# Optimization experiments

Hardware: AMD Instinct MI355X
Metric: run time of the kernel (lower is better)

## Reference

```python
import jax, jax.numpy as jnp
import numpy as np


def setup_inputs() -> dict:
    key = jax.random.key(0)
    ks = jax.random.split(key, 32)
    def rn(i, shape, s=0.02):
        return jax.random.normal(ks[i], shape, dtype=jnp.float32) * s
    z = lambda n: jnp.zeros((n,), dtype=jnp.float32)
    return {
        'c2': rn(0, (8, 256, 112, 112), 1.0),
        'c3': rn(1, (8, 512, 56, 56), 1.0),
        'c4': rn(2, (8, 1024, 28, 28), 1.0),
        'c5': rn(3, (8, 2048, 14, 14), 1.0),
        'lat_w0': rn(4, (256, 256)),  'lat_b0': z(256),
        'lat_w1': rn(5, (512, 256)),  'lat_b1': z(256),
        'lat_w2': rn(6, (1024, 256)), 'lat_b2': z(256),
        'lat_w3': rn(7, (2048, 256)), 'lat_b3': z(256),
        'sp_w1': rn(8, (2048, 512)), 'sp_b1': z(512),
        'sp_w2': rn(9, (512, 4)),    'sp_b2': z(4),
        'qkv_w': rn(10, (256, 768)), 'qkv_b': z(768),
        'proj_w': rn(11, (256, 256)), 'proj_b': z(256),
        'gat_W': rn(12, (4, 256, 256)),
        'gat_a': rn(13, (4, 512)),
        'out_w': rn(14, (1024, 256)), 'out_b': z(256),
        'label_emb': rn(15, (80, 256), 1.0),
        'spec_w1': rn(16, (256, 128)), 'spec_b1': z(128),
        'spec_w2': rn(17, (128, 80)),  'spec_b2': z(80),
        'spat_w1': rn(18, (256, 128)), 'spat_b1': z(128),
        'spat_w2': rn(19, (128, 80)),  'spat_b2': z(80),
        'gate_w': rn(20, (256, 80)), 'gate_b': z(80),
        'unc_w': rn(21, (256, 80)),  'unc_b': z(80),
    }


def _forward(c2, c3, c4, c5,
             lat_w0, lat_b0, lat_w1, lat_b1, lat_w2, lat_b2, lat_w3, lat_b3,
             sp_w1, sp_b1, sp_w2, sp_b2,
             qkv_w, qkv_b, proj_w, proj_b,
             gat_W, gat_a, out_w, out_b, label_emb,
             spec_w1, spec_b1, spec_w2, spec_b2,
             spat_w1, spat_b1, spat_w2, spat_b2,
             gate_w, gate_b, unc_w, unc_b):
    B = c2.shape[0]
    L = label_emb.shape[0]
    C = 256
    # --- DynamicScaleAwareFPN ---
    pooled = c5.mean(axis=(2, 3))                                   # [B,2048]
    sw = jax.nn.softmax(jax.nn.relu(pooled @ sp_w1 + sp_b1) @ sp_w2 + sp_b2, axis=1)  # [B,4]
    H, W = c2.shape[2], c2.shape[3]
    feats = (c2, c3, c4, c5)
    lws = (lat_w0, lat_w1, lat_w2, lat_w3)
    lbs = (lat_b0, lat_b1, lat_b2, lat_b3)
    fused = jnp.zeros((B, C, H, W), dtype=c2.dtype)
    for i in range(4):  # fixed 4 scales
        l = jnp.einsum('bchw,cd->bdhw', feats[i], lws[i]) + lbs[i][None, :, None, None]
        if l.shape[2] != H or l.shape[3] != W:
            l = jax.image.resize(l, (B, C, H, W), method='bilinear')  # align_corners=False
        fused = fused + l * sw[:, i, None, None, None]
    # --- DeformableAttention (N=H*W > max_tokens=196 -> adaptive pool to 14x14) ---
    th = 14
    x = fused.reshape(B, C, th, H // th, th, W // th).mean(axis=(3, 5))  # exact adaptive avg pool
    x = x.reshape(B, C, th * th).transpose(0, 2, 1)                      # [B,196,C]
    N, nh, hd = th * th, 8, C // 8
    qkv = (x @ qkv_w + qkv_b).reshape(B, N, 3, nh, hd).transpose(2, 0, 3, 1, 4)
    q, k, v = qkv[0], qkv[1], qkv[2]                                     # [B,nh,N,hd]
    attn = jax.nn.softmax(jnp.einsum('bhnd,bhmd->bhnm', q, k) * (hd ** -0.5), axis=-1)
    xo = jnp.einsum('bhnm,bhmd->bhnd', attn, v).transpose(0, 2, 1, 3).reshape(B, N, C)
    xo = xo @ proj_w + proj_b
    gctx = xo.mean(axis=1)                                               # [B,C]
    # --- CrossLabelSemanticGraph (4 GAT heads) ---
    lf = label_emb[None] + gctx[:, None, :]                              # [B,L,C]
    def gat(Wm, avec):
        Wx = lf @ Wm                                                     # [B,L,C]
        # a([Wx_i ; Wx_j]) = Wx_i @ a1 + Wx_j @ a2  (avoids O(L^2*2C) tensor)
        s1 = Wx @ avec[:C]                                               # [B,L]
        s2 = Wx @ avec[C:]                                               # [B,L]
        e = jax.nn.leaky_relu(s1[:, :, None] + s2[:, None, :], 0.2)      # [B,L,L]
        att = jax.nn.softmax(e, axis=2)
        return att @ Wx, att
    heads, atts = jax.vmap(gat)(gat_W, gat_a)                            # [4,B,L,C],[4,B,L,L]
    concat = jnp.moveaxis(heads, 0, 2).reshape(B, L, 4 * C)              # head-order concat
    graph = concat @ out_w + out_b                                       # [B,L,C]
    agg = graph.mean(axis=1)                                             # [B,C]
    # --- SpectralSpatialFusion (dropout inactive at eval) ---
    spec = jax.nn.relu(agg @ spec_w1 + spec_b1) @ spec_w2 + spec_b2
    spat = jax.nn.relu(agg @ spat_w1 + spat_b1) @ spat_w2 + spat_b2
    gate = jax.nn.sigmoid(agg @ gate_w + gate_b)
    logits = gate * spec + (1.0 - gate) * spat
    # --- UncertaintyHead ---
    alpha = jax.nn.softplus(agg @ unc_w + unc_b) + 1.0
    unc = L / jnp.sum(alpha, axis=1, keepdims=True)
    return (logits, spec, spat, gate, unc, sw, atts)


def reference(c2, c3, c4, c5,
              lat_w0, lat_b0, lat_w1, lat_b1, lat_w2, lat_b2, lat_w3, lat_b3,
              sp_w1, sp_b1, sp_w2, sp_b2,
              qkv_w, qkv_b, proj_w, proj_b,
              gat_W, gat_a, out_w, out_b, label_emb,
              spec_w1, spec_b1, spec_w2, spec_b2,
              spat_w1, spat_b1, spat_w2, spat_b2,
              gate_w, gate_b, unc_w, unc_b):
    return _forward(c2, c3, c4, c5,
                    lat_w0, lat_b0, lat_w1, lat_b1, lat_w2, lat_b2, lat_w3, lat_b3,
                    sp_w1, sp_b1, sp_w2, sp_b2,
                    qkv_w, qkv_b, proj_w, proj_b,
                    gat_W, gat_a, out_w, out_b, label_emb,
                    spec_w1, spec_b1, spec_w2, spec_b2,
                    spat_w1, spat_b1, spat_w2, spat_b2,
                    gate_w, gate_b, unc_w, unc_b)
```

## Files before the change

kernel.cpp:

```cpp
#include <hip/hip_runtime.h>
#include <math.h>

typedef __attribute__((ext_vector_type(8))) short bshort8;
typedef __attribute__((ext_vector_type(4))) float f32x4;

#define DI __device__ __forceinline__

DI unsigned short f2bf(float x) {
    unsigned int u = __builtin_bit_cast(unsigned int, x);
    u += 0x7fffu + ((u >> 16) & 1u);
    return (unsigned short)(u >> 16);
}

DI bshort8 pack8(const float* v) {
    bshort8 r;
    #pragma unroll
    for (int j = 0; j < 8; j++) r[j] = (short)f2bf(v[j]);
    return r;
}

DI f32x4 mfma16(bshort8 a, bshort8 b, f32x4 c) {
    return __builtin_amdgcn_mfma_f32_16x16x32_bf16(a, b, c, 0, 0, 0);
}

__device__ const float W14[14][3] = {
    {0.875f, 0.125f, 0.f},
    {0.125f, 0.75f, 0.125f}, {0.125f, 0.75f, 0.125f}, {0.125f, 0.75f, 0.125f},
    {0.125f, 0.75f, 0.125f}, {0.125f, 0.75f, 0.125f}, {0.125f, 0.75f, 0.125f},
    {0.125f, 0.75f, 0.125f}, {0.125f, 0.75f, 0.125f}, {0.125f, 0.75f, 0.125f},
    {0.125f, 0.75f, 0.125f}, {0.125f, 0.75f, 0.125f}, {0.125f, 0.75f, 0.125f},
    {0.125f, 0.875f, 0.f}};
__device__ const float W28[14][4] = {
    {0.5f, 0.4375f, 0.0625f, 0.f},
    {0.0625f, 0.4375f, 0.4375f, 0.0625f}, {0.0625f, 0.4375f, 0.4375f, 0.0625f},
    {0.0625f, 0.4375f, 0.4375f, 0.0625f}, {0.0625f, 0.4375f, 0.4375f, 0.0625f},
    {0.0625f, 0.4375f, 0.4375f, 0.0625f}, {0.0625f, 0.4375f, 0.4375f, 0.0625f},
    {0.0625f, 0.4375f, 0.4375f, 0.0625f}, {0.0625f, 0.4375f, 0.4375f, 0.0625f},
    {0.0625f, 0.4375f, 0.4375f, 0.0625f}, {0.0625f, 0.4375f, 0.4375f, 0.0625f},
    {0.0625f, 0.4375f, 0.4375f, 0.0625f}, {0.0625f, 0.4375f, 0.4375f, 0.0625f},
    {0.0625f, 0.4375f, 0.5f, 0.f}};
__device__ const float W56[14][6] = {
    {0.25f, 0.25f, 0.25f, 0.21875f, 0.03125f, 0.f},
    {0.03125f, 0.21875f, 0.25f, 0.25f, 0.21875f, 0.03125f},
    {0.03125f, 0.21875f, 0.25f, 0.25f, 0.21875f, 0.03125f},
    {0.03125f, 0.21875f, 0.25f, 0.25f, 0.21875f, 0.03125f},
    {0.03125f, 0.21875f, 0.25f, 0.25f, 0.21875f, 0.03125f},
    {0.03125f, 0.21875f, 0.25f, 0.25f, 0.21875f, 0.03125f},
    {0.03125f, 0.21875f, 0.25f, 0.25f, 0.21875f, 0.03125f},
    {0.03125f, 0.21875f, 0.25f, 0.25f, 0.21875f, 0.03125f},
    {0.03125f, 0.21875f, 0.25f, 0.25f, 0.21875f, 0.03125f},
    {0.03125f, 0.21875f, 0.25f, 0.25f, 0.21875f, 0.03125f},
    {0.03125f, 0.21875f, 0.25f, 0.25f, 0.21875f, 0.03125f},
    {0.03125f, 0.21875f, 0.25f, 0.25f, 0.21875f, 0.03125f},
    {0.03125f, 0.21875f, 0.25f, 0.25f, 0.21875f, 0.03125f},
    {0.03125f, 0.21875f, 0.25f, 0.25f, 0.25f, 0.f}};

template <int N, int C, int TAPS>
DI void pool_body(const float* __restrict__ src, float* __restrict__ dst,
                  unsigned blk, unsigned t)
{
    unsigned id = blk * 256u + t;
    unsigned p = id / 196u;
    unsigned r = id - p * 196u;
    unsigned ti = r / 14u, tj = r - ti * 14u;
    unsigned b = p / C, cin = p - b * C;
    const float* plane = src + (size_t)p * (N * N);
    float acc = 0.f;
    if constexpr (N == 112) {
        const float4* p4 = (const float4*)(plane + (size_t)(ti * 8) * 112 + tj * 8);
        #pragma unroll
        for (int i = 0; i < 8; i++) {
            float4 u = p4[i * 28];
            float4 v = p4[i * 28 + 1];
            acc += (u.x + u.y) + (u.z + u.w) + (v.x + v.y) + (v.z + v.w);
        }
        acc *= (1.f / 64.f);
    } else {
        constexpr int STRIDE = N / 14;
        const float (*WT)[TAPS] = (N == 14) ? (const float (*)[TAPS])W14
                                : (N == 28) ? (const float (*)[TAPS])W28
                                            : (const float (*)[TAPS])W56;
        int hs = (int)(STRIDE * ti) - 1; if (hs < 0) hs = 0;
        int ws = (int)(STRIDE * tj) - 1; if (ws < 0) ws = 0;
        float wh[TAPS], ww[TAPS];
        #pragma unroll
        for (int i = 0; i < TAPS; i++) { wh[i] = WT[ti][i]; ww[i] = WT[tj][i]; }
        #pragma unroll
        for (int i = 0; i < TAPS; i++) {
            int hi = hs + i; if (hi > N - 1) hi = N - 1;
            const float* row = plane + (size_t)hi * N;
            float rs = 0.f;
            #pragma unroll
            for (int j = 0; j < TAPS; j++) {
                int wj = ws + j; if (wj > N - 1) wj = N - 1;
                rs += ww[j] * row[wj];
            }
            acc += wh[i] * rs;
        }
    }
    dst[(size_t)cin * 1568 + b * 196 + r] = acc;
}

DI void c5_mean_body(const float* __restrict__ c5, float* __restrict__ pooled,
                     unsigned blk, unsigned t)
{
    int wid = t >> 6, lane = t & 63;
    int p = blk * 4 + wid;
    const float* plane = c5 + (size_t)p * 196;
    float v = plane[lane] + plane[64 + lane] + plane[128 + lane];
    if (lane < 4) v += plane[192 + lane];
    #pragma unroll
    for (int off = 32; off > 0; off >>= 1) v += __shfl_xor(v, off, 64);
    if (lane == 0) pooled[p] = v * (1.f / 196.f);
}

__global__ __launch_bounds__(256) void pool_all(
    const float* __restrict__ c2, const float* __restrict__ c3,
    const float* __restrict__ c4, const float* __restrict__ c5,
    float* __restrict__ pf0, float* __restrict__ pf1,
    float* __restrict__ pf2, float* __restrict__ pf3,
    float* __restrict__ pooled)
{
    unsigned bx = blockIdx.x, t = threadIdx.x;
    if (bx < 1568u)       pool_body<112, 256, 8>(c2, pf0, bx, t);
    else if (bx < 4704u)  pool_body<56, 512, 6>(c3, pf1, bx - 1568u, t);
    else if (bx < 10976u) pool_body<28, 1024, 4>(c4, pf2, bx - 4704u, t);
    else if (bx < 23520u) pool_body<14, 2048, 3>(c5, pf3, bx - 10976u, t);
    else                  c5_mean_body(c5, pooled, bx - 23520u, t);
}

__global__ __launch_bounds__(512) void sw_part(
    const float* __restrict__ pooled, const float* __restrict__ sp_w1,
    float* __restrict__ partial,
    const float* __restrict__ gat_W, const float* __restrict__ gat_a,
    float* __restrict__ Wa)
{
    int t = threadIdx.x;
    if (blockIdx.y >= 8) {
        int e = (blockIdx.y - 8) * 8 + blockIdx.x;
        int h = e >> 2, q = e & 3;
        __shared__ float a1[256], a2[256];
        if (t < 256) { a1[t] = gat_a[h * 512 + t]; a2[t] = gat_a[h * 512 + 256 + t]; }
        __syncthreads();
        int w = t >> 6, lane = t & 63;
        #pragma unroll
        for (int ci = 0; ci < 8; ci++) {
            int c = q * 64 + w * 8 + ci;
            const float* row = gat_W + (size_t)h * 65536 + (size_t)c * 256;
            float p1 = 0.f, p2 = 0.f;
            #pragma unroll
            for (int jj = 0; jj < 4; jj++) {
                float v = row[lane + 64 * jj];
                p1 += v * a1[lane + 64 * jj];
                p2 += v * a2[lane + 64 * jj];
            }
            #pragma unroll
            for (int off = 32; off > 0; off >>= 1) {
                p1 += __shfl_xor(p1, off, 64);
                p2 += __shfl_xor(p2, off, 64);
            }
            if (lane == 0) { Wa[h * 512 + c] = p1; Wa[h * 512 + 256 + c] = p2; }
        }
        return;
    }
    int b = blockIdx.x, kc = blockIdx.y;
    __shared__ float ps[256];
    if (t < 256) ps[t] = pooled[b * 2048 + kc * 256 + t];
    __syncthreads();
    float acc = 0.f;
    const float* w = sp_w1 + (size_t)(kc * 256) * 512 + t;
    #pragma unroll 8
    for (int c = 0; c < 256; c++) acc += ps[c] * w[(size_t)c * 512];
    partial[((size_t)b * 8 + kc) * 512 + t] = acc;
}

__global__ __launch_bounds__(512) void sw_fin(
    const float* __restrict__ partial, const float* __restrict__ sp_b1,
    const float* __restrict__ sp_w2, const float* __restrict__ sp_b2,
    const float* __restrict__ lb0, const float* __restrict__ lb1,
    const float* __restrict__ lb2, const float* __restrict__ lb3,
    const float* __restrict__ lemb, const float* __restrict__ Wa,
    float* __restrict__ sw_out, float* __restrict__ xtok,
    float* __restrict__ ldot)
{
    int b = blockIdx.x, t = threadIdx.x;
    __shared__ float h[512];
    __shared__ float s4s[4];
    __shared__ float swl[4];
    __shared__ float bf_s[256];
    float a = sp_b1[t];
    #pragma unroll
    for (int kc = 0; kc < 8; kc++) a += partial[((size_t)b * 8 + kc) * 512 + t];
    h[t] = fmaxf(a, 0.f);
    __syncthreads();
    int wv = t >> 6, lane = t & 63;
    if (wv < 4) {
        float acc = 0.f;
        #pragma unroll
        for (int i = 0; i < 8; i++) {
            int idx = lane + 64 * i;
            acc += h[idx] * sp_w2[idx * 4 + wv];
        }
        #pragma unroll
        for (int off = 32; off > 0; off >>= 1) acc += __shfl_xor(acc, off, 64);
        if (lane == 0) s4s[wv] = acc + sp_b2[wv];
    }
    __syncthreads();
    if (t == 0) {
        float mx = fmaxf(fmaxf(s4s[0], s4s[1]), fmaxf(s4s[2], s4s[3]));
        float e0 = expf(s4s[0] - mx), e1 = expf(s4s[1] - mx);
        float e2 = expf(s4s[2] - mx), e3 = expf(s4s[3] - mx);
        float inv = 1.f / (e0 + e1 + e2 + e3);
        swl[0] = e0 * inv; swl[1] = e1 * inv; swl[2] = e2 * inv; swl[3] = e3 * inv;
        for (int o = 0; o < 4; o++) sw_out[b * 4 + o] = swl[o];
    }
    __syncthreads();
    if (t < 256)
        bf_s[t] = swl[0] * lb0[t] + swl[1] * lb1[t] + swl[2] * lb2[t] + swl[3] * lb3[t];
    {
        int pair = t >> 6;
        #pragma unroll
        for (int r = 0; r < 10; r++) {
            int l = b * 10 + r;
            const float* le = lemb + l * 256 + lane * 4;
            const float* wa = Wa + pair * 256 + lane * 4;
            float p = le[0] * wa[0] + le[1] * wa[1] + le[2] * wa[2] + le[3] * wa[3];
            #pragma unroll
            for (int off = 32; off > 0; off >>= 1) p += __shfl_xor(p, off, 64);
            if (lane == 0) ldot[l * 8 + pair] = p;
        }
    }
    __syncthreads();
    int c = t & 255, half = t >> 8;
    float bv = bf_s[c];
    float* xb = xtok + (size_t)b * 196 * 256 + c;
    for (int r = half; r < 196; r += 2) xb[(size_t)r * 256] = bv;
}

__global__ __launch_bounds__(256) void lateral_slice(
    const float* __restrict__ pf0, const float* __restrict__ pf1,
    const float* __restrict__ pf2, const float* __restrict__ pf3,
    const float* __restrict__ w0, const float* __restrict__ w1,
    const float* __restrict__ w2, const float* __restrict__ w3,
    const float* __restrict__ sw, float* __restrict__ xtok)
{
    const int sArr[8]    = {0, 1, 2, 2, 3, 3, 3, 3};
    const int koffArr[8] = {0, 0, 0, 512, 0, 512, 1024, 1536};
    const int klenArr[8] = {256, 512, 512, 512, 512, 512, 512, 512};
    int sl = blockIdx.y;
    int s = sArr[sl], koff = koffArr[sl], klen = klenArr[sl];
    const float* pf = (s == 0) ? pf0 : (s == 1) ? pf1 : (s == 2) ? pf2 : pf3;
    const float* W  = (s == 0) ? w0  : (s == 1) ? w1  : (s == 2) ? w2  : w3;

    int mt = blockIdx.x % 49, nt = blockIdx.x / 49;
    int m0 = mt * 32, n0 = nt * 64;
    __shared__ alignas(16) unsigned short As[1024];
    __shared__ alignas(16) unsigned short Bs[2048];
    int t = threadIdx.x, lane = t & 63, wid = t >> 6;
    int wm = wid >> 1, wn = wid & 1;
    f32x4 acc0 = {0, 0, 0, 0}, acc1 = {0, 0, 0, 0};

    int f = t & 63;
    int mA = m0 + ((t >> 6) & 1) * 16 + (f & 15);
    int kbA = (f >> 4) * 8;
    int nB = n0 + (t >> 6) * 16 + (f & 15);
    int kbB = (f >> 4) * 8;
    float swv = sw[(mA / 196) * 4 + s];

    float ar[8], br[8];
    auto loadA = [&](int k0) {
        if (t < 128) {
            const float* base = pf + (size_t)(koff + k0 + kbA) * 1568 + mA;
            #pragma unroll
            for (int j = 0; j < 8; j++) ar[j] = base[(size_t)j * 1568] * swv;
        }
    };
    auto loadB = [&](int k0) {
        const float* base = W + (size_t)(koff + k0 + kbB) * 256 + nB;
        #pragma unroll
        for (int j = 0; j < 8; j++) br[j] = base[(size_t)j * 256];
    };

    loadA(0); loadB(0);
    for (int k0 = 0; k0 < klen; k0 += 32) {
        if (t < 128) *(bshort8*)&As[(((t >> 6) & 1) * 512 + f * 8)] = pack8(ar);
        *(bshort8*)&Bs[((t >> 6) * 512 + f * 8)] = pack8(br);
        __syncthreads();
        if (k0 + 32 < klen) { loadA(k0 + 32); loadB(k0 + 32); }
        bshort8 av = *(const bshort8*)&As[wm * 512 + lane * 8];
        bshort8 bv0 = *(const bshort8*)&Bs[(wn * 2 + 0) * 512 + lane * 8];
        bshort8 bv1 = *(const bshort8*)&Bs[(wn * 2 + 1) * 512 + lane * 8];
        acc0 = mfma16(av, bv0, acc0);
        acc1 = mfma16(av, bv1, acc1);
        __syncthreads();
    }
    int col0 = n0 + wn * 32 + (lane & 15);
    int rbase = m0 + wm * 16 + ((lane >> 4) << 2);
    #pragma unroll
    for (int r = 0; r < 4; r++) {
        int m = rbase + r;
        atomicAdd(&xtok[(size_t)m * 256 + col0], acc0[r]);
        atomicAdd(&xtok[(size_t)m * 256 + col0 + 16], acc1[r]);
    }
}

template <bool B_IS_KXN>
__global__ __launch_bounds__(256) void gemm_kernel(
    const float* __restrict__ Ab, int lda, long long sAy, long long sAz,
    const float* __restrict__ Bb, int ldb, long long sBy, long long sBz,
    float* __restrict__ Cb, int ldc, long long sCy, long long sCz,
    const float* __restrict__ bias, int M, int N, int K,
    float alpha, int mtiles)
{
    const float* A = Ab + blockIdx.y * sAy + blockIdx.z * sAz;
    const float* B = Bb + blockIdx.y * sBy + blockIdx.z * sBz;
    float* C = Cb + blockIdx.y * sCy + blockIdx.z * sCz;
    int mt = blockIdx.x % mtiles, nt = blockIdx.x / mtiles;
    int m0 = mt * 32, n0 = nt * 64;
    __shared__ alignas(16) unsigned short As[1024];
    __shared__ alignas(16) unsigned short Bs[2048];
    int t = threadIdx.x, lane = t & 63, wid = t >> 6;
    int wm = wid >> 1, wn = wid & 1;
    f32x4 acc0 = {0, 0, 0, 0}, acc1 = {0, 0, 0, 0};

    int f = t & 63;
    int mA = m0 + ((t >> 6) & 1) * 16 + (f & 15);
    int kbA = (f >> 4) * 8;
    int nB = n0 + (t >> 6) * 16 + (f & 15);
    int kbB = (f >> 4) * 8;

    float ar[8], br[8];
    auto loadA = [&](int k0) {
        if (t < 128) {
            int kb = k0 + kbA;
            if (mA < M && kb + 8 <= K) {
                const float4* p = (const float4*)(A + (size_t)mA * lda + kb);
                float4 u = p[0], v = p[1];
                ar[0] = u.x; ar[1] = u.y; ar[2] = u.z; ar[3] = u.w;
                ar[4] = v.x; ar[5] = v.y; ar[6] = v.z; ar[7] = v.w;
            } else {
                #pragma unroll
                for (int j = 0; j < 8; j++) {
                    int k = kb + j;
                    ar[j] = (mA < M && k < K) ? A[(size_t)mA * lda + k] : 0.f;
                }
            }
        }
    };
    auto loadB = [&](int k0) {
        int kb = k0 + kbB;
        if constexpr (B_IS_KXN) {
            #pragma unroll
            for (int j = 0; j < 8; j++) {
                int k = kb + j;
                br[j] = (k < K && nB < N) ? B[(size_t)k * ldb + nB] : 0.f;
            }
        } else {
            if (nB < N && kb + 8 <= K) {
                const float4* p = (const float4*)(B + (size_t)nB * ldb + kb);
                float4 u = p[0], v = p[1];
                br[0] = u.x; br[1] = u.y; br[2] = u.z; br[3] = u.w;
                br[4] = v.x; br[5] = v.y; br[6] = v.z; br[7] = v.w;
            } else {
                #pragma unroll
                for (int j = 0; j < 8; j++) {
                    int k = kb + j;
                    br[j] = (nB < N && k < K) ? B[(size_t)nB * ldb + k] : 0.f;
                }
            }
        }
    };

    loadA(0); loadB(0);
    for (int k0 = 0; k0 < K; k0 += 32) {
        if (t < 128) *(bshort8*)&As[(((t >> 6) & 1) * 512 + f * 8)] = pack8(ar);
        *(bshort8*)&Bs[((t >> 6) * 512 + f * 8)] = pack8(br);
        __syncthreads();
        if (k0 + 32 < K) { loadA(k0 + 32); loadB(k0 + 32); }
        bshort8 av = *(const bshort8*)&As[wm * 512 + lane * 8];
        bshort8 bv0 = *(const bshort8*)&Bs[(wn * 2 + 0) * 512 + lane * 8];
        bshort8 bv1 = *(const bshort8*)&Bs[(wn * 2 + 1) * 512 + lane * 8];
        acc0 = mfma16(av, bv0, acc0);
        acc1 = mfma16(av, bv1, acc1);
        __syncthreads();
    }
    int col0 = n0 + wn * 32 + (lane & 15);
    int rbase = m0 + wm * 16 + ((lane >> 4) << 2);
    #pragma unroll
    for (int r = 0; r < 4; r++) {
        int m = rbase + r;
        if (m < M) {
            if (col0 < N) {
                float v = acc0[r] * alpha;
                if (bias) v += bias[col0];
                C[(size_t)m * ldc + col0] = v;
            }
            int c1 = col0 + 16;
            if (c1 < N) {
                float v = acc1[r] * alpha;
                if (bias) v += bias[c1];
                C[(size_t)m * ldc + c1] = v;
            }
        }
    }
}

__global__ __launch_bounds__(256) void attn_softmax(float* __restrict__ S)
{
    int wid = threadIdx.x >> 6, lane = threadIdx.x & 63;
    size_t row = (size_t)blockIdx.x * 4 + wid;
    float* p = S + row * 196;
    float v0 = p[lane];
    float v1 = p[64 + lane];
    float v2 = p[128 + lane];
    float v3 = (lane < 4) ? p[192 + lane] : -1e30f;
    float mx = fmaxf(fmaxf(v0, v1), fmaxf(v2, v3));
    #pragma unroll
    for (int off = 32; off > 0; off >>= 1) mx = fmaxf(mx, __shfl_xor(mx, off, 64));
    float e0 = expf(v0 - mx), e1 = expf(v1 - mx), e2 = expf(v2 - mx);
    float e3 = (lane < 4) ? expf(v3 - mx) : 0.f;
    float sum = e0 + e1 + e2 + e3;
    #pragma unroll
    for (int off = 32; off > 0; off >>= 1) sum += __shfl_xor(sum, off, 64);
    float inv = 1.f / sum;
    p[lane] = e0 * inv;
    p[64 + lane] = e1 * inv;
    p[128 + lane] = e2 * inv;
    if (lane < 4) p[192 + lane] = e3 * inv;
}

__global__ __launch_bounds__(1024) void tail1(
    const float* __restrict__ xo, const float* __restrict__ proj_w,
    const float* __restrict__ proj_b,
    const float* __restrict__ gat_W, const float* __restrict__ lemb,
    const float* __restrict__ Wa, const float* __restrict__ ldot,
    float* __restrict__ atts, float* __restrict__ hm_g)
{
    int b = blockIdx.x >> 2, h = blockIdx.x & 3;
    int t = threadIdx.x, lane = t & 63, wv = t >> 6;
    __shared__ float red[1024];
    __shared__ float xm[256];
    __shared__ float gctx_s[256];
    __shared__ float gdot_s[2];
    __shared__ float s12h[160];
    __shared__ float am_s[80];
    __shared__ float av_s[256];

    {
        int c = t & 255, sl = t >> 8;
        const float* base = xo + ((size_t)b * 196 + sl * 49) * 256 + c;
        float s = 0.f;
        #pragma unroll 7
        for (int i = 0; i < 49; i++) s += base[(size_t)i * 256];
        red[t] = s;
    }
    if (t < 80) am_s[t] = 0.f;
    __syncthreads();
    if (t < 256) xm[t] = (red[t] + red[256 + t] + red[512 + t] + red[768 + t]) * (1.f / 196.f);
    __syncthreads();

    {
        int n = t & 255, ks = t >> 8;
        float acc = 0.f;
        const float* w = proj_w + (size_t)(ks * 64) * 256 + n;
        #pragma unroll 8
        for (int i = 0; i < 64; i++) acc += xm[ks * 64 + i] * w[(size_t)i * 256];
        red[t] = acc;
    }
    __syncthreads();
    if (t < 256) gctx_s[t] = proj_b[t] + red[t] + red[256 + t] + red[512 + t] + red[768 + t];
    __syncthreads();

    if (wv < 2) {
        int pair = h * 2 + wv;
        const float* wa = Wa + pair * 256 + lane * 4;
        float p = gctx_s[lane * 4] * wa[0] + gctx_s[lane * 4 + 1] * wa[1]
                + gctx_s[lane * 4 + 2] * wa[2] + gctx_s[lane * 4 + 3] * wa[3];
        #pragma unroll
        for (int off = 32; off > 0; off >>= 1) p += __shfl_xor(p, off, 64);
        if (lane == 0) gdot_s[wv] = p;
    }
    __syncthreads();
    if (t < 160) {
        int q = t / 80, l = t - q * 80;
        s12h[t] = ldot[l * 8 + h * 2 + q] + gdot_s[q];
    }
    __syncthreads();

    {
        #pragma unroll
        for (int rr = 0; rr < 5; rr++) {
            int i = rr * 16 + wv;
            float s1i = s12h[i];
            const float* s2 = s12h + 80;
            float v0 = s1i + s2[lane]; v0 = v0 > 0.f ? v0 : 0.2f * v0;
            float v1 = -1e30f;
            if (lane < 16) { v1 = s1i + s2[64 + lane]; v1 = v1 > 0.f ? v1 : 0.2f * v1; }
            float mx = fmaxf(v0, v1);
            #pragma unroll
            for (int off = 32; off > 0; off >>= 1) mx = fmaxf(mx, __shfl_xor(mx, off, 64));
            float e0 = expf(v0 - mx), e1 = (lane < 16) ? expf(v1 - mx) : 0.f;
            float sum = e0 + e1;
            #pragma unroll
            for (int off = 32; off > 0; off >>= 1) sum += __shfl_xor(sum, off, 64);
            float inv = 1.f / sum;
            float* orow = atts + (size_t)h * 51200 + b * 6400 + i * 80;
            float p0 = e0 * inv;
            orow[lane] = p0;
            atomicAdd(&am_s[lane], p0);
            if (lane < 16) {
                float p1 = e1 * inv;
                orow[64 + lane] = p1;
                atomicAdd(&am_s[64 + lane], p1);
            }
        }
    }
    __syncthreads();

    {
        int n = t & 255, ks = t >> 8;
        float acc = 0.f;
        const float* le = lemb + n;
        #pragma unroll 5
        for (int l = ks * 20; l < ks * 20 + 20; l++) acc += am_s[l] * le[(size_t)l * 256];
        red[t] = acc;
    }
    __syncthreads();
    if (t < 256)
        av_s[t] = (red[t] + red[256 + t] + red[512 + t] + red[768 + t]) * (1.f / 80.f)
                + gctx_s[t];
    __syncthreads();
    {
        int n = t & 255, ks = t >> 8;
        float acc = 0.f;
        const float* w = gat_W + (size_t)h * 65536 + (size_t)(ks * 64) * 256 + n;
        #pragma unroll 8
        for (int i = 0; i < 64; i++) acc += av_s[ks * 64 + i] * w[(size_t)i * 256];
        red[t] = acc;
    }
    __syncthreads();
    if (t < 256)
        hm_g[(b * 4 + h) * 256 + t] = red[t] + red[256 + t] + red[512 + t] + red[768 + t];
}

__global__ __launch_bounds__(1024) void tail2(
    const float* __restrict__ hm_g,
    const float* __restrict__ out_w, const float* __restrict__ out_b,
    const float* __restrict__ spec_w1, const float* __restrict__ spec_b1,
    const float* __restrict__ spec_w2, const float* __restrict__ spec_b2,
    const float* __restrict__ spat_w1, const float* __restrict__ spat_b1,
    const float* __restrict__ spat_w2, const float* __restrict__ spat_b2,
    const float* __restrict__ gate_w, const float* __restrict__ gate_b,
    const float* __restrict__ unc_w, const float* __restrict__ unc_b,
    float* __restrict__ out)
{
    int b = blockIdx.x, t = threadIdx.x;
    __shared__ float red[1024];
    __shared__ float as_s[256];
    __shared__ float hb_s[256];
    __shared__ float fv_s[320];

    {
        int n = t & 255, ks = t >> 8;
        float acc = 0.f;
        const float* hv = hm_g + b * 1024 + ks * 256;
        const float* w = out_w + (size_t)(ks * 256) * 256 + n;
        #pragma unroll 8
        for (int k = 0; k < 256; k++) acc += hv[k] * w[(size_t)k * 256];
        red[t] = acc;
    }
    __syncthreads();
    if (t < 256) as_s[t] = out_b[t] + red[t] + red[256 + t] + red[512 + t] + red[768 + t];
    __syncthreads();

    {
        int u = t & 255, ks = t >> 8;
        int which = u >> 7, oo = u & 127;
        const float* w1 = which ? spat_w1 : spec_w1;
        float acc = 0.f;
        #pragma unroll 8
        for (int i = 0; i < 64; i++) {
            int k = ks * 64 + i;
            acc += as_s[k] * w1[(size_t)k * 128 + oo];
        }
        red[t] = acc;
    }
    __syncthreads();
    if (t < 256) {
        int which = t >> 7, oo = t & 127;
        const float* b1 = which ? spat_b1 : spec_b1;
        hb_s[t] = fmaxf(red[t] + red[256 + t] + red[512 + t] + red[768 + t] + b1[oo], 0.f);
    }
    __syncthreads();

    if (t < 960) {
        int sub = t / 320, u = t - sub * 320;
        int head = u / 80, o = u - head * 80;
        const float* wp; const float* src; int K;
        if (head == 0)      { wp = spec_w2; src = hb_s;       K = 128; }
        else if (head == 1) { wp = spat_w2; src = hb_s + 128; K = 128; }
        else if (head == 2) { wp = gate_w;  src = as_s;       K = 256; }
        else                { wp = unc_w;   src = as_s;       K = 256; }
        int k0 = (K * sub) / 3, k1 = (K * (sub + 1)) / 3;
        float acc = 0.f;
        for (int k = k0; k < k1; k++) acc += src[k] * wp[(size_t)k * 80 + o];
        red[sub * 320 + u] = acc;
    }
    __syncthreads();
    if (t < 320) {
        int head = t / 80, o = t - head * 80;
        const float* bp = head == 0 ? spec_b2 : head == 1 ? spat_b2 : head == 2 ? gate_b : unc_b;
        fv_s[t] = red[t] + red[320 + t] + red[640 + t] + bp[o];
    }
    __syncthreads();

    if (t < 80) {
        float sp = fv_s[t], st2 = fv_s[80 + t], gz = fv_s[160 + t], uz = fv_s[240 + t];
        float g = 1.f / (1.f + expf(-gz));
        out[b * 80 + t] = g * sp + (1.f - g) * st2;
        out[640 + b * 80 + t] = sp;
        out[1280 + b * 80 + t] = st2;
        out[1920 + b * 80 + t] = g;
        red[t] = log1pf(expf(uz)) + 1.f;
    }
    __syncthreads();
    if (t == 0) {
        float s = 0.f;
        for (int l = 0; l < 80; l++) s += red[l];
        out[2560 + b] = 80.f / s;
    }
}

extern "C" void kernel_launch(void* const* d_in, const int* in_sizes, int n_in,
                              void* d_out, int out_size, void* d_ws, size_t ws_size,
                              hipStream_t stream)
{
    (void)in_sizes; (void)n_in; (void)out_size; (void)ws_size;
    const float* c2 = (const float*)d_in[0];
    const float* c3 = (const float*)d_in[1];
    const float* c4 = (const float*)d_in[2];
    const float* c5 = (const float*)d_in[3];
    const float* lat_w0 = (const float*)d_in[4];
    const float* lat_b0 = (const float*)d_in[5];
    const float* lat_w1 = (const float*)d_in[6];
    const float* lat_b1 = (const float*)d_in[7];
    const float* lat_w2 = (const float*)d_in[8];
    const float* lat_b2 = (const float*)d_in[9];
    const float* lat_w3 = (const float*)d_in[10];
    const float* lat_b3 = (const float*)d_in[11];
    const float* sp_w1 = (const float*)d_in[12];
    const float* sp_b1 = (const float*)d_in[13];
    const float* sp_w2 = (const float*)d_in[14];
    const float* sp_b2 = (const float*)d_in[15];
    const float* qkv_w = (const float*)d_in[16];
    const float* qkv_b = (const float*)d_in[17];
    const float* proj_w = (const float*)d_in[18];
    const float* proj_b = (const float*)d_in[19];
    const float* gat_W = (const float*)d_in[20];
    const float* gat_a = (const float*)d_in[21];
    const float* out_w = (const float*)d_in[22];
    const float* out_b = (const float*)d_in[23];
    const float* label_emb = (const float*)d_in[24];
    const float* spec_w1 = (const float*)d_in[25];
    const float* spec_b1 = (const float*)d_in[26];
    const float* spec_w2 = (const float*)d_in[27];
    const float* spec_b2 = (const float*)d_in[28];
    const float* spat_w1 = (const float*)d_in[29];
    const float* spat_b1 = (const float*)d_in[30];
    const float* spat_w2 = (const float*)d_in[31];
    const float* spat_b2 = (const float*)d_in[32];
    const float* gate_w = (const float*)d_in[33];
    const float* gate_b = (const float*)d_in[34];
    const float* unc_w = (const float*)d_in[35];
    const float* unc_b = (const float*)d_in[36];

    float* out = (float*)d_out;
    float* ws = (float*)d_ws;

    float* pf0    = ws + 0;
    float* pf1    = ws + 401408;
    float* pf2    = ws + 1204224;
    float* pf3    = ws + 2809856;
    float* pooled = ws + 6021120;
    float* swpart = ws + 6039552;
    float* Wa     = ws + 6072320;
    float* ldot   = ws + 6074368;
    float* qkv    = ws + 0;
    float* S      = ws + 1204224;
    float* xo     = ws + 3662848;
    float* hm_g   = ws + 4253696;
    float* xtok   = ws + 6106112;

    float* swp  = out + 2568;
    float* atts = out + 2600;

    pool_all<<<27616, 256, 0, stream>>>(c2, c3, c4, c5, pf0, pf1, pf2, pf3, pooled);
    sw_part<<<dim3(8, 10), 512, 0, stream>>>(pooled, sp_w1, swpart, gat_W, gat_a, Wa);
    sw_fin<<<8, 512, 0, stream>>>(swpart, sp_b1, sp_w2, sp_b2,
                                  lat_b0, lat_b1, lat_b2, lat_b3,
                                  label_emb, Wa, swp, xtok, ldot);
    lateral_slice<<<dim3(196, 8), 256, 0, stream>>>(pf0, pf1, pf2, pf3,
                                                    lat_w0, lat_w1, lat_w2, lat_w3,
                                                    swp, xtok);
    gemm_kernel<true><<<dim3(49 * 12, 1, 1), 256, 0, stream>>>(
        xtok, 256, 0, 0, qkv_w, 768, 0, 0, qkv, 768, 0, 0,
        qkv_b, 1568, 768, 256, 1.f, 49);
    gemm_kernel<false><<<dim3(7 * 4, 8, 8), 256, 0, stream>>>(
        qkv, 768, 150528, 32, qkv + 256, 768, 150528, 32,
        S, 196, 307328, 38416, nullptr, 196, 196, 32, 0.17677669529663687f, 7);
    attn_softmax<<<3136, 256, 0, stream>>>(S);
    gemm_kernel<true><<<dim3(7, 8, 8), 256, 0, stream>>>(
        S, 196, 307328, 38416, qkv + 512, 768, 150528, 32,
        xo, 256, 50176, 32, nullptr, 196, 32, 196, 1.f, 7);
    tail1<<<32, 1024, 0, stream>>>(xo, proj_w, proj_b, gat_W, label_emb,
                                   Wa, ldot, atts, hm_g);
    tail2<<<8, 1024, 0, stream>>>(hm_g, out_w, out_b,
                                  spec_w1, spec_b1, spec_w2, spec_b2,
                                  spat_w1, spat_b1, spat_w2, spat_b2,
                                  gate_w, gate_b, unc_w, unc_b, out);
}
```

Before: 507.2 us.

## Fuse attention into one kernel and store pooled features as bf16

Measured after the change: 494.1 us. 2.6% less time.

```diff
diff --git a/kernel.cpp b/kernel.cpp
--- a/kernel.cpp
+++ b/kernel.cpp
@@ -56,7 +56,7 @@
     {0.03125f, 0.21875f, 0.25f, 0.25f, 0.25f, 0.f}};
 
 template <int N, int C, int TAPS>
-DI void pool_body(const float* __restrict__ src, float* __restrict__ dst,
+DI void pool_body(const float* __restrict__ src, unsigned short* __restrict__ dst,
                   unsigned blk, unsigned t)
 {
     unsigned id = blk * 256u + t;
@@ -68,12 +68,11 @@
     float acc = 0.f;
     if constexpr (N == 112) {
         const float4* p4 = (const float4*)(plane + (size_t)(ti * 8) * 112 + tj * 8);
-        #pragma unroll
-        for (int i = 0; i < 8; i++) {
-            float4 u = p4[i * 28];
-            float4 v = p4[i * 28 + 1];
-            acc += (u.x + u.y) + (u.z + u.w) + (v.x + v.y) + (v.z + v.w);
-        }
+        float4 rv[16];
+        #pragma unroll
+        for (int i = 0; i < 8; i++) { rv[2 * i] = p4[i * 28]; rv[2 * i + 1] = p4[i * 28 + 1]; }
+        #pragma unroll
+        for (int i = 0; i < 16; i++) acc += (rv[i].x + rv[i].y) + (rv[i].z + rv[i].w);
         acc *= (1.f / 64.f);
     } else {
         constexpr int STRIDE = N / 14;
@@ -85,20 +84,26 @@
         float wh[TAPS], ww[TAPS];
         #pragma unroll
         for (int i = 0; i < TAPS; i++) { wh[i] = WT[ti][i]; ww[i] = WT[tj][i]; }
+        float rv[TAPS][TAPS];
         #pragma unroll
         for (int i = 0; i < TAPS; i++) {
             int hi = hs + i; if (hi > N - 1) hi = N - 1;
             const float* row = plane + (size_t)hi * N;
-            float rs = 0.f;
             #pragma unroll
             for (int j = 0; j < TAPS; j++) {
                 int wj = ws + j; if (wj > N - 1) wj = N - 1;
-                rs += ww[j] * row[wj];
-            }
+                rv[i][j] = row[wj];
+            }
+        }
+        #pragma unroll
+        for (int i = 0; i < TAPS; i++) {
+            float rs = 0.f;
+            #pragma unroll
+            for (int j = 0; j < TAPS; j++) rs += ww[j] * rv[i][j];
             acc += wh[i] * rs;
         }
     }
-    dst[(size_t)cin * 1568 + b * 196 + r] = acc;
+    dst[(size_t)cin * 1568 + b * 196 + r] = f2bf(acc);
 }
 
 DI void c5_mean_body(const float* __restrict__ c5, float* __restrict__ pooled,
@@ -117,8 +122,8 @@
 __global__ __launch_bounds__(256) void pool_all(
     const float* __restrict__ c2, const float* __restrict__ c3,
     const float* __restrict__ c4, const float* __restrict__ c5,
-    float* __restrict__ pf0, float* __restrict__ pf1,
-    float* __restrict__ pf2, float* __restrict__ pf3,
+    unsigned short* __restrict__ pf0, unsigned short* __restrict__ pf1,
+    unsigned short* __restrict__ pf2, unsigned short* __restrict__ pf3,
     float* __restrict__ pooled)
 {
     unsigned bx = blockIdx.x, t = threadIdx.x;
@@ -238,8 +243,8 @@
 }
 
 __global__ __launch_bounds__(256) void lateral_slice(
-    const float* __restrict__ pf0, const float* __restrict__ pf1,
-    const float* __restrict__ pf2, const float* __restrict__ pf3,
+    const unsigned short* __restrict__ pf0, const unsigned short* __restrict__ pf1,
+    const unsigned short* __restrict__ pf2, const unsigned short* __restrict__ pf3,
     const float* __restrict__ w0, const float* __restrict__ w1,
     const float* __restrict__ w2, const float* __restrict__ w3,
     const float* __restrict__ sw, float* __restrict__ xtok)
@@ -249,7 +254,7 @@
     const int klenArr[8] = {256, 512, 512, 512, 512, 512, 512, 512};
     int sl = blockIdx.y;
     int s = sArr[sl], koff = koffArr[sl], klen = klenArr[sl];
-    const float* pf = (s == 0) ? pf0 : (s == 1) ? pf1 : (s == 2) ? pf2 : pf3;
+    const unsigned short* pf = (s == 0) ? pf0 : (s == 1) ? pf1 : (s == 2) ? pf2 : pf3;
     const float* W  = (s == 0) ? w0  : (s == 1) ? w1  : (s == 2) ? w2  : w3;
 
     int mt = blockIdx.x % 49, nt = blockIdx.x / 49;
@@ -265,14 +270,14 @@
     int kbA = (f >> 4) * 8;
     int nB = n0 + (t >> 6) * 16 + (f & 15);
     int kbB = (f >> 4) * 8;
-    float swv = sw[(mA / 196) * 4 + s];
-
-    float ar[8], br[8];
+
+    unsigned short ark[8];
+    float br[8];
     auto loadA = [&](int k0) {
         if (t < 128) {
-            const float* base = pf + (size_t)(koff + k0 + kbA) * 1568 + mA;
-            #pragma unroll
-            for (int j = 0; j < 8; j++) ar[j] = base[(size_t)j * 1568] * swv;
+            const unsigned short* base = pf + (size_t)(koff + k0 + kbA) * 1568 + mA;
+            #pragma unroll
+            for (int j = 0; j < 8; j++) ark[j] = base[(size_t)j * 1568];
         }
     };
     auto loadB = [&](int k0) {
@@ -283,7 +288,12 @@
 
     loadA(0); loadB(0);
     for (int k0 = 0; k0 < klen; k0 += 32) {
-        if (t < 128) *(bshort8*)&As[(((t >> 6) & 1) * 512 + f * 8)] = pack8(ar);
+        if (t < 128) {
+            bshort8 v8;
+            #pragma unroll
+            for (int j = 0; j < 8; j++) v8[j] = (short)ark[j];
+            *(bshort8*)&As[(((t >> 6) & 1) * 512 + f * 8)] = v8;
+        }
         *(bshort8*)&Bs[((t >> 6) * 512 + f * 8)] = pack8(br);
         __syncthreads();
         if (k0 + 32 < klen) { loadA(k0 + 32); loadB(k0 + 32); }
@@ -299,8 +309,9 @@
     #pragma unroll
     for (int r = 0; r < 4; r++) {
         int m = rbase + r;
-        atomicAdd(&xtok[(size_t)m * 256 + col0], acc0[r]);
-        atomicAdd(&xtok[(size_t)m * 256 + col0 + 16], acc1[r]);
+        float swv = sw[(m / 196) * 4 + s];
+        atomicAdd(&xtok[(size_t)m * 256 + col0], acc0[r] * swv);
+        atomicAdd(&xtok[(size_t)m * 256 + col0 + 16], acc1[r] * swv);
     }
 }
 
@@ -405,28 +416,148 @@
     }
 }
 
-__global__ __launch_bounds__(256) void attn_softmax(float* __restrict__ S)
-{
-    int wid = threadIdx.x >> 6, lane = threadIdx.x & 63;
-    size_t row = (size_t)blockIdx.x * 4 + wid;
-    float* p = S + row * 196;
-    float v0 = p[lane];
-    float v1 = p[64 + lane];
-    float v2 = p[128 + lane];
-    float v3 = (lane < 4) ? p[192 + lane] : -1e30f;
-    float mx = fmaxf(fmaxf(v0, v1), fmaxf(v2, v3));
-    #pragma unroll
-    for (int off = 32; off > 0; off >>= 1) mx = fmaxf(mx, __shfl_xor(mx, off, 64));
-    float e0 = expf(v0 - mx), e1 = expf(v1 - mx), e2 = expf(v2 - mx);
-    float e3 = (lane < 4) ? expf(v3 - mx) : 0.f;
-    float sum = e0 + e1 + e2 + e3;
-    #pragma unroll
-    for (int off = 32; off > 0; off >>= 1) sum += __shfl_xor(sum, off, 64);
-    float inv = 1.f / sum;
-    p[lane] = e0 * inv;
-    p[64 + lane] = e1 * inv;
-    p[128 + lane] = e2 * inv;
-    if (lane < 4) p[192 + lane] = e3 * inv;
+__global__ __launch_bounds__(256) void fused_attn(
+    const float* __restrict__ qkv, float* __restrict__ xo)
+{
+    int mt = blockIdx.x, h = blockIdx.y, b = blockIdx.z;
+    const float* Qb = qkv + (size_t)b * 150528 + h * 32;
+    const float* Kb = Qb + 256;
+    const float* Vb = Qb + 512;
+
+    __shared__ alignas(16) unsigned short As[1024];
+    __shared__ alignas(16) unsigned short Bs[2048];
+    __shared__ float Ss[32 * 256];
+
+    int t = threadIdx.x, lane = t & 63, wid = t >> 6;
+    int wm = wid >> 1, wn = wid & 1;
+    int f = t & 63;
+    int m0 = mt * 32;
+
+    if (t < 128) {
+        float ar[8];
+        int mA = m0 + ((t >> 6) & 1) * 16 + (f & 15);
+        int kb = (f >> 4) * 8;
+        if (mA < 196) {
+            const float4* p = (const float4*)(Qb + (size_t)mA * 768 + kb);
+            float4 u = p[0], v = p[1];
+            ar[0] = u.x; ar[1] = u.y; ar[2] = u.z; ar[3] = u.w;
+            ar[4] = v.x; ar[5] = v.y; ar[6] = v.z; ar[7] = v.w;
+        } else {
+            #pragma unroll
+            for (int j = 0; j < 8; j++) ar[j] = 0.f;
+        }
+        *(bshort8*)&As[(((t >> 6) & 1) * 512 + f * 8)] = pack8(ar);
+    }
+
+    {
+        int nBl = (t >> 6) * 16 + (f & 15);
+        int kbB = (f >> 4) * 8;
+        float br[8];
+        auto loadB = [&](int g) {
+            int key = g * 64 + nBl;
+            if (key < 196) {
+                const float4* p = (const float4*)(Kb + (size_t)key * 768 + kbB);
+                float4 u = p[0], v = p[1];
+                br[0] = u.x; br[1] = u.y; br[2] = u.z; br[3] = u.w;
+                br[4] = v.x; br[5] = v.y; br[6] = v.z; br[7] = v.w;
+            } else {
+                #pragma unroll
+                for (int j = 0; j < 8; j++) br[j] = 0.f;
+            }
+        };
+        loadB(0);
+        for (int g = 0; g < 4; g++) {
+            __syncthreads();
+            *(bshort8*)&Bs[((t >> 6) * 512 + f * 8)] = pack8(br);
+            __syncthreads();
+            if (g < 3) loadB(g + 1);
+            f32x4 acc0 = {0, 0, 0, 0}, acc1 = {0, 0, 0, 0};
+            bshort8 av = *(const bshort8*)&As[wm * 512 + lane * 8];
+            bshort8 bv0 = *(const bshort8*)&Bs[(wn * 2 + 0) * 512 + lane * 8];
+            bshort8 bv1 = *(const bshort8*)&Bs[(wn * 2 + 1) * 512 + lane * 8];
+            acc0 = mfma16(av, bv0, acc0);
+            acc1 = mfma16(av, bv1, acc1);
+            int col0 = g * 64 + wn * 32 + (lane & 15);
+            int rbase = wm * 16 + ((lane >> 4) << 2);
+            #pragma unroll
+            for (int r = 0; r < 4; r++) {
+                Ss[(rbase + r) * 256 + col0]      = acc0[r] * 0.17677669529663687f;
+                Ss[(rbase + r) * 256 + col0 + 16] = acc1[r] * 0.17677669529663687f;
+            }
+        }
+    }
+    __syncthreads();
+
+    {
+        #pragma unroll
+        for (int i = 0; i < 8; i++) {
+            float* p = Ss + (wid * 8 + i) * 256;
+            float v0 = p[lane], v1 = p[64 + lane], v2 = p[128 + lane];
+            float v3 = (lane < 4) ? p[192 + lane] : -1e30f;
+            float mx = fmaxf(fmaxf(v0, v1), fmaxf(v2, v3));
+            #pragma unroll
+            for (int off = 32; off > 0; off >>= 1) mx = fmaxf(mx, __shfl_xor(mx, off, 64));
+            float e0 = expf(v0 - mx), e1 = expf(v1 - mx), e2 = expf(v2 - mx);
+            float e3 = (lane < 4) ? expf(v3 - mx) : 0.f;
+            float sum = e0 + e1 + e2 + e3;
+            #pragma unroll
+            for (int off = 32; off > 0; off >>= 1) sum += __shfl_xor(sum, off, 64);
+            float inv = 1.f / sum;
+            p[lane] = e0 * inv;
+            p[64 + lane] = e1 * inv;
+            p[128 + lane] = e2 * inv;
+            if (lane < 4) p[192 + lane] = e3 * inv;
+            else          p[192 + lane] = 0.f;
+        }
+    }
+    __syncthreads();
+
+    {
+        f32x4 acc0 = {0, 0, 0, 0}, acc1 = {0, 0, 0, 0};
+        int nBl = (t >> 6) * 16 + (f & 15);
+        int kbB = (f >> 4) * 8;
+        int mAl = ((t >> 6) & 1) * 16 + (f & 15);
+        int kbA = (f >> 4) * 8;
+        float ar[8], br[8];
+        auto loadA = [&](int k0) {
+            if (t < 128) {
+                #pragma unroll
+                for (int j = 0; j < 8; j++) ar[j] = Ss[mAl * 256 + k0 + kbA + j];
+            }
+        };
+        auto loadB = [&](int k0) {
+            #pragma unroll
+            for (int j = 0; j < 8; j++) {
+                int k = k0 + kbB + j;
+                br[j] = (k < 196 && nBl < 32) ? Vb[(size_t)k * 768 + nBl] : 0.f;
+            }
+        };
+        loadA(0); loadB(0);
+        for (int k0 = 0; k0 < 256; k0 += 32) {
+            __syncthreads();
+            if (t < 128) *(bshort8*)&As[(((t >> 6) & 1) * 512 + f * 8)] = pack8(ar);
+            *(bshort8*)&Bs[((t >> 6) * 512 + f * 8)] = pack8(br);
+            __syncthreads();
+            if (k0 + 32 < 256) { loadA(k0 + 32); loadB(k0 + 32); }
+            bshort8 av = *(const bshort8*)&As[wm * 512 + lane * 8];
+            bshort8 bv0 = *(const bshort8*)&Bs[(wn * 2 + 0) * 512 + lane * 8];
+            bshort8 bv1 = *(const bshort8*)&Bs[(wn * 2 + 1) * 512 + lane * 8];
+            acc0 = mfma16(av, bv0, acc0);
+            acc1 = mfma16(av, bv1, acc1);
+        }
+        int col0 = wn * 32 + (lane & 15);
+        int rbase = wm * 16 + ((lane >> 4) << 2);
+        if (col0 < 32) {
+            #pragma unroll
+            for (int r = 0; r < 4; r++) {
+                int m = m0 + rbase + r;
+                if (m < 196) {
+                    xo[((size_t)b * 196 + m) * 256 + h * 32 + col0]      = acc0[r];
+                    xo[((size_t)b * 196 + m) * 256 + h * 32 + col0 + 16] = acc1[r];
+                }
+            }
+        }
+    }
 }
 
 __global__ __launch_bounds__(1024) void tail1(
@@ -677,16 +808,15 @@
     float* out = (float*)d_out;
     float* ws = (float*)d_ws;
 
-    float* pf0    = ws + 0;
-    float* pf1    = ws + 401408;
-    float* pf2    = ws + 1204224;
-    float* pf3    = ws + 2809856;
+    unsigned short* pf0 = (unsigned short*)(ws + 0);
+    unsigned short* pf1 = (unsigned short*)(ws + 401408);
+    unsigned short* pf2 = (unsigned short*)(ws + 1204224);
+    unsigned short* pf3 = (unsigned short*)(ws + 2809856);
     float* pooled = ws + 6021120;
     float* swpart = ws + 6039552;
     float* Wa     = ws + 6072320;
     float* ldot   = ws + 6074368;
     float* qkv    = ws + 0;
-    float* S      = ws + 1204224;
     float* xo     = ws + 3662848;
     float* hm_g   = ws + 4253696;
     float* xtok   = ws + 6106112;
@@ -705,13 +835,7 @@
     gemm_kernel<true><<<dim3(49 * 12, 1, 1), 256, 0, stream>>>(
         xtok, 256, 0, 0, qkv_w, 768, 0, 0, qkv, 768, 0, 0,
         qkv_b, 1568, 768, 256, 1.f, 49);
-    gemm_kernel<false><<<dim3(7 * 4, 8, 8), 256, 0, stream>>>(
-        qkv, 768, 150528, 32, qkv + 256, 768, 150528, 32,
-        S, 196, 307328, 38416, nullptr, 196, 196, 32, 0.17677669529663687f, 7);
-    attn_softmax<<<3136, 256, 0, stream>>>(S);
-    gemm_kernel<true><<<dim3(7, 8, 8), 256, 0, stream>>>(
-        S, 196, 307328, 38416, qkv + 512, 768, 150528, 32,
-        xo, 256, 50176, 32, nullptr, 196, 32, 196, 1.f, 7);
+    fused_attn<<<dim3(7, 8, 8), 256, 0, stream>>>(qkv, xo);
     tail1<<<32, 1024, 0, stream>>>(xo, proj_w, proj_b, gat_W, label_emb,
                                    Wa, ldot, atts, hm_g);
     tail2<<<8, 1024, 0, stream>>>(hm_g, out_w, out_b,
```
